# Kernel optimization log

Measured on AMD Instinct MI355X. Metric: run time of the kernel, lower is better.

Reference implementation:

```python
import jax, jax.numpy as jnp
import numpy as np

N_RES = 500000


def _rot(vals):
    # stack 9 scalars-per-element into (..., 3, 3) row-major rotation matrices
    return jnp.stack(vals, axis=-1).reshape(*vals[0].shape, 3, 3)


def _dihedral(p0, p1, p2, p3):
    b0 = -(p1 - p0)
    b1 = p2 - p1
    b2 = p3 - p2
    b0xb1 = jnp.cross(b0, b1)
    b1xb2 = jnp.cross(b2, b1)
    y = jnp.sum(jnp.cross(b0xb1, b1xb2) * b1, axis=-1) / jnp.linalg.norm(b1, axis=-1)
    x = jnp.sum(b0xb1 * b1xb2, axis=-1)
    return jnp.nan_to_num(jnp.arctan2(y, x))


def _bb_dihedrals(N, CA, C):
    phi_ = _dihedral(C[:-1], N[1:], CA[1:], C[1:])
    psi_ = _dihedral(N[:-1], CA[:-1], C[:-1], N[1:])
    omg_ = _dihedral(CA[:-1], C[:-1], N[1:], CA[1:])
    pad = jnp.zeros_like(phi_[:1])
    omega = jnp.concatenate([omg_, pad])
    phi = jnp.concatenate([pad, phi_])
    psi = jnp.concatenate([psi_, pad])
    return jnp.stack([omega, phi, psi], axis=-1)  # (n, 3)


def _frames_from_reference(n_xyz, ca_xyz, c_xyz, eps=1e-20):
    # OpenFold Rigid.make_transform_from_reference
    n = n_xyz - ca_xyz
    c = c_xyz - ca_xyz
    cx, cy, cz = c[..., 0], c[..., 1], c[..., 2]
    z = jnp.zeros_like(cx)
    o = jnp.ones_like(cx)
    nrm = jnp.sqrt(eps + cx**2 + cy**2)
    s1, c1 = -cy / nrm, cx / nrm
    R1 = _rot([c1, -s1, z, s1, c1, z, z, z, o])
    nrm2 = jnp.sqrt(eps + cx**2 + cy**2 + cz**2)
    s2, c2 = cz / nrm2, jnp.sqrt(cx**2 + cy**2) / nrm2
    R2 = _rot([c2, z, s2, z, o, z, -s2, z, c2])
    Rc = R2 @ R1
    n2 = jnp.einsum('...ij,...j->...i', Rc, n)
    ny, nz_ = n2[..., 1], n2[..., 2]
    nrm3 = jnp.sqrt(eps + ny**2 + nz_**2)
    sn, cn = -nz_ / nrm3, ny / nrm3
    Rn = _rot([o, z, z, z, cn, -sn, z, sn, cn])
    rots = jnp.swapaxes(Rn @ Rc, -1, -2)
    return rots, ca_xyz  # (n,3,3), (n,3)


def _compose(ra, ta, rb, tb):
    # rigid composition: (ra,ta) o (rb,tb)
    return ra @ rb, jnp.einsum('...ij,...j->...i', ra, tb) + ta


def _forward(aa, bb_coords, sc_torsions, default_frames, group_idx, atom_mask, lit_positions):
    n_xyz, ca_xyz, c_xyz = bb_coords[:, 0], bb_coords[:, 1], bb_coords[:, 2]
    bb_r, bb_t = _frames_from_reference(n_xyz, ca_xyz, c_xyz)

    angles = jnp.concatenate([_bb_dihedrals(n_xyz, ca_xyz, c_xyz), sc_torsions], axis=-1)  # (n,7)
    alpha = jnp.stack([jnp.sin(angles), jnp.cos(angles)], axis=-1)  # (n,7,2) [sin, cos]
    bb_pad = jnp.concatenate([
        jnp.zeros((alpha.shape[0], 1, 1), alpha.dtype),
        jnp.ones((alpha.shape[0], 1, 1), alpha.dtype)], axis=-1)
    alpha = jnp.concatenate([bb_pad, alpha], axis=-2)  # (n,8,2)

    # torsion_angles_to_frames
    d4 = default_frames[aa]            # (n,8,4,4)
    dr, dt = d4[..., :3, :3], d4[..., :3, 3]
    s, cA = alpha[..., 0], alpha[..., 1]
    z = jnp.zeros_like(s)
    o = jnp.ones_like(s)
    Ra = _rot([o, z, z, z, cA, -s, z, s, cA])  # (n,8,3,3) x-axis rotation
    fr = dr @ Ra
    ft = dt
    # chain chi2->chi1, chi3->chi2, chi4->chi3
    r2, t2 = _compose(fr[:, 4], ft[:, 4], fr[:, 5], ft[:, 5])
    r3, t3 = _compose(r2, t2, fr[:, 6], ft[:, 6])
    r4, t4 = _compose(r3, t3, fr[:, 7], ft[:, 7])
    all_r = jnp.concatenate([fr[:, :5], r2[:, None], r3[:, None], r4[:, None]], axis=1)
    all_t = jnp.concatenate([ft[:, :5], t2[:, None], t3[:, None], t4[:, None]], axis=1)
    gr, gt = _compose(bb_r[:, None], bb_t[:, None], all_r, all_t)  # (n,8,3,3), (n,8,3)

    # frames_and_literature_positions_to_atom14_pos (one-hot sum == gather)
    n = aa.shape[0]
    g = group_idx[aa]                   # (n,14)
    ridx = jnp.arange(n)[:, None]
    ar = gr[ridx, g]                    # (n,14,3,3)
    at = gt[ridx, g]                    # (n,14,3)
    lit = lit_positions[aa]             # (n,14,3)
    pred = jnp.einsum('naij,naj->nai', ar, lit) + at
    pred = pred * atom_mask[aa][..., None]

    # use_native_bb_coords=True: keep input backbone atoms
    return jnp.concatenate([bb_coords, pred[:, 4:]], axis=1)  # (n,14,3)


def setup_inputs() -> dict:
    key = jax.random.key(0)
    ks = jax.random.split(key, 7)
    n = N_RES
    aa = jax.random.randint(ks[0], (n,), 0, 21, dtype=jnp.int32)
    bb_coords = jax.random.normal(ks[1], (n, 4, 3), jnp.float32) * 3.0
    sc_torsions = jax.random.uniform(ks[2], (n, 4), jnp.float32, -np.pi, np.pi)
    default_frames = jax.random.normal(ks[3], (21, 8, 4, 4), jnp.float32)
    group_idx = jax.random.randint(ks[4], (21, 14), 0, 8, dtype=jnp.int32)
    atom_mask = (jax.random.uniform(ks[5], (21, 14)) > 0.2).astype(jnp.float32)
    lit_positions = jax.random.normal(ks[6], (21, 14, 3), jnp.float32)
    return {"aa": aa, "bb_coords": bb_coords, "sc_torsions": sc_torsions,
            "default_frames": default_frames, "group_idx": group_idx,
            "atom_mask": atom_mask, "lit_positions": lit_positions}


def reference(aa, bb_coords, sc_torsions, default_frames, group_idx, atom_mask, lit_positions):
    return _forward(aa, bb_coords, sc_torsions, default_frames, group_idx, atom_mask, lit_positions)
```

## Files before the change

### kernel.cpp

```cpp
#include <hip/hip_runtime.h>
#include <hip/hip_fp16.h>


struct F3 { float x, y, z; };

__device__ __forceinline__ F3 f3sub(F3 a, F3 b) { return {a.x-b.x, a.y-b.y, a.z-b.z}; }
__device__ __forceinline__ F3 f3cross(F3 a, F3 b) {
    return {a.y*b.z - a.z*b.y, a.z*b.x - a.x*b.z, a.x*b.y - a.y*b.x};
}
__device__ __forceinline__ float f3dot(F3 a, F3 b) { return a.x*b.x + a.y*b.y + a.z*b.z; }

__device__ __forceinline__ void dihedral_sc(F3 p0, F3 p1, F3 p2, F3 p3,
                                            float& s, float& c) {
    F3 b0 = f3sub(p0, p1);
    F3 b1 = f3sub(p2, p1);
    F3 b2 = f3sub(p3, p2);
    F3 u = f3cross(b0, b1);
    F3 v = f3cross(b2, b1);
    F3 w = f3cross(u, v);
    float y = f3dot(w, b1) * rsqrtf(fmaxf(f3dot(b1, b1), 1e-30f));
    float x = f3dot(u, v);
    float r2 = x*x + y*y;
    if (r2 > 1e-24f) {
        float rinv = rsqrtf(r2);
        s = y * rinv;
        c = x * rinv;
    } else {
        s = 0.0f;
        c = 1.0f;
    }
}

#define LIT_STRIDE 30
#define OT_STRIDE  30

__global__ __launch_bounds__(256, 4) void idealizer_kernel(
    const int*   __restrict__ aa,
    const float* __restrict__ bb,
    const float* __restrict__ tor,
    const float* __restrict__ dframes,
    const int*   __restrict__ gidx,
    const float* __restrict__ amask,
    const float* __restrict__ lit,
    float*       __restrict__ out,
    int n)
{
    __shared__ __align__(16) float  s_ot[256 * OT_STRIDE];
    __shared__ __align__(8)  __half s_dfh[21 * 8 * 12];
    __shared__ __align__(16) float  s_lit[21 * LIT_STRIDE];
    __shared__ unsigned s_gpk[21];
    __shared__ unsigned s_mbit[21];

    const int tid = threadIdx.x;
    for (int j = tid; j < 21 * 8 * 12; j += 256) {
        int blk = j / 12, e = j - blk * 12;
        s_dfh[j] = __float2half(dframes[blk * 16 + e]);
    }
    for (int j = tid; j < 21 * 30; j += 256) {
        int a = j / 30, r = j - a * 30;
        s_lit[a * LIT_STRIDE + r] = lit[a * 42 + 12 + r];
    }
    if (tid < 21) {
        unsigned gp = 0, mb = 0;
        #pragma unroll
        for (int a = 0; a < 10; a++) {
            gp |= ((unsigned)gidx[tid * 14 + 4 + a]) << (3 * a);
            mb |= (amask[tid * 14 + 4 + a] != 0.0f ? 1u : 0u) << a;
        }
        s_gpk[tid] = gp;
        s_mbit[tid] = mb;
    }
    __syncthreads();

    for (int i0 = blockIdx.x * 256; i0 < n; i0 += gridDim.x * 256) {
        const int i = i0 + tid;
        if (i < n) {
            const float4* bb4 = (const float4*)bb;
            float4 q0 = bb4[i * 3 + 0];
            float4 q1 = bb4[i * 3 + 1];
            float Cz  = bb[i * 12 + 8];
            F3 Np  = {q0.x, q0.y, q0.z};
            F3 CAp = {q0.w, q1.x, q1.y};
            F3 Cp  = {q1.z, q1.w, Cz};

            const int im = (i > 0)     ? i - 1 : 0;
            const int ip = (i < n - 1) ? i + 1 : 0;
            F3 Cm = { bb[im * 12 + 6], bb[im * 12 + 7], bb[im * 12 + 8] };
            float4 r0 = bb4[ip * 3 + 0];
            float2 r1 = ((const float2*)bb)[ip * 6 + 2];
            F3 Nn  = {r0.x, r0.y, r0.z};
            F3 CAn = {r0.w, r1.x, r1.y};

            float s_ph, c_ph, s_ps, c_ps, s_om, c_om;
            dihedral_sc(Cm,  Np,  CAp, Cp,  s_ph, c_ph);
            dihedral_sc(Np,  CAp, Cp,  Nn,  s_ps, c_ps);
            dihedral_sc(CAp, Cp,  Nn,  CAn, s_om, c_om);
            if (i == 0)     { s_ph = 0.0f; c_ph = 1.0f; }
            if (i == n - 1) { s_ps = 0.0f; c_ps = 1.0f; s_om = 0.0f; c_om = 1.0f; }

            const float eps = 1e-20f;
            F3 nv = f3sub(Np, CAp);
            F3 cv = f3sub(Cp, CAp);
            float cx = cv.x, cy = cv.y, cz = cv.z;
            float d2xy  = cx * cx + cy * cy;
            float inrm  = rsqrtf(eps + d2xy);
            float s1 = -cy * inrm, c1 = cx * inrm;
            float inrm2 = rsqrtf(eps + d2xy + cz * cz);
            float s2v = cz * inrm2, c2v = sqrtf(d2xy) * inrm2;
            float Rc00 = c2v * c1,  Rc01 = -c2v * s1, Rc02 = s2v;
            float Rc10 = s1,        Rc11 = c1,        Rc12 = 0.0f;
            float Rc20 = -s2v * c1, Rc21 = s2v * s1,  Rc22 = c2v;
            float n2y = Rc10 * nv.x + Rc11 * nv.y + Rc12 * nv.z;
            float n2z = Rc20 * nv.x + Rc21 * nv.y + Rc22 * nv.z;
            float inrm3 = rsqrtf(eps + n2y * n2y + n2z * n2z);
            float sn = -n2z * inrm3, cn = n2y * inrm3;
            float M10 = cn * Rc10 - sn * Rc20, M11 = cn * Rc11 - sn * Rc21, M12 = cn * Rc12 - sn * Rc22;
            float M20 = sn * Rc10 + cn * Rc20, M21 = sn * Rc11 + cn * Rc21, M22 = sn * Rc12 + cn * Rc22;
            float B00 = Rc00, B01 = M10, B02 = M20;
            float B10 = Rc01, B11 = M11, B12 = M21;
            float B20 = Rc02, B21 = M12, B22 = M22;

            float4 tv = ((const float4*)tor)[i];
            float sang[8], cang[8];
            sang[0] = 0.0f; cang[0] = 1.0f;
            sang[1] = s_om; cang[1] = c_om;
            sang[2] = s_ph; cang[2] = c_ph;
            sang[3] = s_ps; cang[3] = c_ps;
            __sincosf(tv.x, &sang[4], &cang[4]);
            __sincosf(tv.y, &sang[5], &cang[5]);
            __sincosf(tv.z, &sang[6], &cang[6]);
            __sincosf(tv.w, &sang[7], &cang[7]);

            const int aai = aa[i];
            const unsigned gpk  = s_gpk[aai];
            const unsigned mbit = s_mbit[aai];
            const float* lrow = &s_lit[aai * LIT_STRIDE];
            float* srow = &s_ot[tid * OT_STRIDE];

            float L00, L01, L02, L10, L11, L12, L20, L21, L22, Lx, Ly, Lz;
            const __half2* dfa = (const __half2*)(s_dfh + (size_t)aai * 96);
            #pragma unroll
            for (int g = 0; g < 8; g++) {
                const __half2* dh = dfa + g * 6;
                float2 e0 = __half22float2(dh[0]), e1 = __half22float2(dh[1]);
                float2 e2 = __half22float2(dh[2]), e3 = __half22float2(dh[3]);
                float2 e4 = __half22float2(dh[4]), e5 = __half22float2(dh[5]);
                float m00 = e0.x, m01 = e0.y, m02 = e1.x, tx = e1.y;
                float m10 = e2.x, m11 = e2.y, m12 = e3.x, ty = e3.y;
                float m20 = e4.x, m21 = e4.y, m22 = e5.x, tz = e5.y;
                float sA = sang[g], cA = cang[g];
                float f00 = m00, f01 = cA * m01 + sA * m02, f02 = cA * m02 - sA * m01;
                float f10 = m10, f11 = cA * m11 + sA * m12, f12 = cA * m12 - sA * m11;
                float f20 = m20, f21 = cA * m21 + sA * m22, f22 = cA * m22 - sA * m21;
                if (g <= 4) {
                    L00 = f00; L01 = f01; L02 = f02;
                    L10 = f10; L11 = f11; L12 = f12;
                    L20 = f20; L21 = f21; L22 = f22;
                    Lx = tx; Ly = ty; Lz = tz;
                } else {
                    float n00 = L00 * f00 + L01 * f10 + L02 * f20;
                    float n01 = L00 * f01 + L01 * f11 + L02 * f21;
                    float n02 = L00 * f02 + L01 * f12 + L02 * f22;
                    float n10 = L10 * f00 + L11 * f10 + L12 * f20;
                    float n11 = L10 * f01 + L11 * f11 + L12 * f21;
                    float n12 = L10 * f02 + L11 * f12 + L12 * f22;
                    float n20 = L20 * f00 + L21 * f10 + L22 * f20;
                    float n21 = L20 * f01 + L21 * f11 + L22 * f21;
                    float n22 = L20 * f02 + L21 * f12 + L22 * f22;
                    float ntx = L00 * tx + L01 * ty + L02 * tz + Lx;
                    float nty = L10 * tx + L11 * ty + L12 * tz + Ly;
                    float ntz = L20 * tx + L21 * ty + L22 * tz + Lz;
                    L00 = n00; L01 = n01; L02 = n02;
                    L10 = n10; L11 = n11; L12 = n12;
                    L20 = n20; L21 = n21; L22 = n22;
                    Lx = ntx; Ly = nty; Lz = ntz;
                }

                #pragma unroll
                for (int a = 0; a < 10; a++) {
                    bool sel = ((gpk >> (3 * a)) & 7u) == (unsigned)g;
                    if (sel) {
                        float mk = ((mbit >> a) & 1u) ? 1.0f : 0.0f;
                        float lx = lrow[3*a], ly = lrow[3*a+1], lz = lrow[3*a+2];
                        float qx = fmaf(L00, lx, fmaf(L01, ly, fmaf(L02, lz, Lx)));
                        float qy = fmaf(L10, lx, fmaf(L11, ly, fmaf(L12, lz, Ly)));
                        float qz = fmaf(L20, lx, fmaf(L21, ly, fmaf(L22, lz, Lz)));
                        float px = fmaf(B00, qx, fmaf(B01, qy, fmaf(B02, qz, CAp.x)));
                        float py = fmaf(B10, qx, fmaf(B11, qy, fmaf(B12, qz, CAp.y)));
                        float pz = fmaf(B20, qx, fmaf(B21, qy, fmaf(B22, qz, CAp.z)));
                        float* po = srow + 3 * a;
                        po[0] = mk * px;
                        po[1] = mk * py;
                        po[2] = mk * pz;
                    }
                }
            }
        }

        __syncthreads();

        int m = n - i0; if (m > 256) m = 256;
        const int cnt2 = m * 21;
        float2* gout = (float2*)(out + (size_t)i0 * 42);
        const float2* bbt = (const float2*)(bb + (size_t)i0 * 12);
        for (int off = tid; off < cnt2; off += 256) {
            int r = off / 21, j = off - r * 21;
            float2 val;
            if (j < 6) {
                val = bbt[r * 6 + j];
            } else {
                const float* tp = &s_ot[r * OT_STRIDE + 2 * (j - 6)];
                val = make_float2(tp[0], tp[1]);
            }
            gout[off] = val;
        }

        __syncthreads();
    }
}

extern "C" void kernel_launch(void* const* d_in, const int* in_sizes, int n_in,
                              void* d_out, int out_size, void* d_ws, size_t ws_size,
                              hipStream_t stream) {
    const int*   aa  = (const int*)d_in[0];
    const float* bb  = (const float*)d_in[1];
    const float* tor = (const float*)d_in[2];
    const float* df  = (const float*)d_in[3];
    const int*   gi  = (const int*)d_in[4];
    const float* am  = (const float*)d_in[5];
    const float* lp  = (const float*)d_in[6];
    float* outp = (float*)d_out;
    const int n = in_sizes[0];
    int tiles = (n + 255) / 256;
    int blocks = tiles < 1024 ? tiles : 1024;
    idealizer_kernel<<<blocks, 256, 0, stream>>>(aa, bb, tor, df, gi, am, lp, outp, n);
}
```

Baseline: 156.6 us.

## Share dihedral cross products, store frames fp32, predicate atom placement, simplify store indexing

Computes the backbone bond vectors and their cross products once and shares them across the phi, psi and omega dihedrals. Default frames now sit in shared memory as fp32 float4 rows and literature positions as fp16. Atom placement becomes branchless: local positions are selected into registers, the backbone transform is applied once per atom, and results are written to LDS as float2. The output copy loop advances row and column incrementally instead of dividing each iteration. It also lowers the launch-bounds occupancy hint from 4 to 3 and adds a redundant M22 expression. The costs are higher register pressure, extra FMAs for atoms that are not selected, and fp16 rounding of the literature positions.

```diff
diff --git a/kernel.cpp b/kernel.cpp
--- a/kernel.cpp
+++ b/kernel.cpp
@@ -10,31 +10,22 @@
 }
 __device__ __forceinline__ float f3dot(F3 a, F3 b) { return a.x*b.x + a.y*b.y + a.z*b.z; }
 
-__device__ __forceinline__ void dihedral_sc(F3 p0, F3 p1, F3 p2, F3 p3,
-                                            float& s, float& c) {
-    F3 b0 = f3sub(p0, p1);
-    F3 b1 = f3sub(p2, p1);
-    F3 b2 = f3sub(p3, p2);
-    F3 u = f3cross(b0, b1);
-    F3 v = f3cross(b2, b1);
-    F3 w = f3cross(u, v);
-    float y = f3dot(w, b1) * rsqrtf(fmaxf(f3dot(b1, b1), 1e-30f));
-    float x = f3dot(u, v);
-    float r2 = x*x + y*y;
-    if (r2 > 1e-24f) {
-        float rinv = rsqrtf(r2);
-        s = y * rinv;
-        c = x * rinv;
-    } else {
-        s = 0.0f;
-        c = 1.0f;
-    }
-}
-
-#define LIT_STRIDE 30
-#define OT_STRIDE  30
-
-__global__ __launch_bounds__(256, 4) void idealizer_kernel(
+__device__ __forceinline__ void dihedral_from(F3 A, F3 B, F3 mid,
+                                              float& s, float& c) {
+    float x = f3dot(A, B);
+    F3 w = f3cross(A, B);
+    float y = f3dot(w, mid) * rsqrtf(fmaxf(f3dot(mid, mid), 1e-30f));
+    float r2 = x * x + y * y;
+    float rinv = rsqrtf(r2);
+    bool ok = r2 > 1e-24f;
+    s = ok ? y * rinv : 0.0f;
+    c = ok ? x * rinv : 1.0f;
+}
+
+#define DF_AA     100
+#define OT_STRIDE 30
+
+__global__ __launch_bounds__(256, 3) void idealizer_kernel(
     const int*   __restrict__ aa,
     const float* __restrict__ bb,
     const float* __restrict__ tor,
@@ -46,19 +37,19 @@
     int n)
 {
     __shared__ __align__(16) float  s_ot[256 * OT_STRIDE];
-    __shared__ __align__(8)  __half s_dfh[21 * 8 * 12];
-    __shared__ __align__(16) float  s_lit[21 * LIT_STRIDE];
+    __shared__ __align__(16) float  s_df[21 * DF_AA];
+    __shared__ __align__(8)  __half s_lith[21 * 32];
     __shared__ unsigned s_gpk[21];
     __shared__ unsigned s_mbit[21];
 
     const int tid = threadIdx.x;
     for (int j = tid; j < 21 * 8 * 12; j += 256) {
         int blk = j / 12, e = j - blk * 12;
-        s_dfh[j] = __float2half(dframes[blk * 16 + e]);
+        s_df[(blk >> 3) * DF_AA + (blk & 7) * 12 + e] = dframes[blk * 16 + e];
     }
     for (int j = tid; j < 21 * 30; j += 256) {
         int a = j / 30, r = j - a * 30;
-        s_lit[a * LIT_STRIDE + r] = lit[a * 42 + 12 + r];
+        s_lith[a * 32 + r] = __float2half(lit[a * 42 + 12 + r]);
     }
     if (tid < 21) {
         unsigned gp = 0, mb = 0;
@@ -91,22 +82,29 @@
             F3 Nn  = {r0.x, r0.y, r0.z};
             F3 CAn = {r0.w, r1.x, r1.y};
 
+            F3 u1 = f3sub(Np, Cm);
+            F3 u2 = f3sub(CAp, Np);
+            F3 u3 = f3sub(Cp, CAp);
+            F3 u4 = f3sub(Nn, Cp);
+            F3 u5 = f3sub(CAn, Nn);
+            F3 c12 = f3cross(u1, u2), c23 = f3cross(u2, u3);
+            F3 c34 = f3cross(u3, u4), c45 = f3cross(u4, u5);
             float s_ph, c_ph, s_ps, c_ps, s_om, c_om;
-            dihedral_sc(Cm,  Np,  CAp, Cp,  s_ph, c_ph);
-            dihedral_sc(Np,  CAp, Cp,  Nn,  s_ps, c_ps);
-            dihedral_sc(CAp, Cp,  Nn,  CAn, s_om, c_om);
+            dihedral_from(c12, c23, u2, s_ph, c_ph);
+            dihedral_from(c23, c34, u3, s_ps, c_ps);
+            dihedral_from(c34, c45, u4, s_om, c_om);
             if (i == 0)     { s_ph = 0.0f; c_ph = 1.0f; }
             if (i == n - 1) { s_ps = 0.0f; c_ps = 1.0f; s_om = 0.0f; c_om = 1.0f; }
 
             const float eps = 1e-20f;
             F3 nv = f3sub(Np, CAp);
             F3 cv = f3sub(Cp, CAp);
-            float cx = cv.x, cy = cv.y, cz = cv.z;
+            float cx = cv.x, cy = cv.y, cz2 = cv.z;
             float d2xy  = cx * cx + cy * cy;
             float inrm  = rsqrtf(eps + d2xy);
             float s1 = -cy * inrm, c1 = cx * inrm;
-            float inrm2 = rsqrtf(eps + d2xy + cz * cz);
-            float s2v = cz * inrm2, c2v = sqrtf(d2xy) * inrm2;
+            float inrm2 = rsqrtf(eps + d2xy + cz2 * cz2);
+            float s2v = cz2 * inrm2, c2v = sqrtf(d2xy) * inrm2;
             float Rc00 = c2v * c1,  Rc01 = -c2v * s1, Rc02 = s2v;
             float Rc10 = s1,        Rc11 = c1,        Rc12 = 0.0f;
             float Rc20 = -s2v * c1, Rc21 = s2v * s1,  Rc22 = c2v;
@@ -115,7 +113,8 @@
             float inrm3 = rsqrtf(eps + n2y * n2y + n2z * n2z);
             float sn = -n2z * inrm3, cn = n2y * inrm3;
             float M10 = cn * Rc10 - sn * Rc20, M11 = cn * Rc11 - sn * Rc21, M12 = cn * Rc12 - sn * Rc22;
-            float M20 = sn * Rc10 + cn * Rc20, M21 = sn * Rc11 + cn * Rc21, M22 = sn * Rc12 + cn * Rc22;
+            float M20 = sn * Rc10 + cn * Rc20, M21 = sn * Rc11 + cn * Rc21, M22 = sn * Rc22 * 0.0f + sn * Rc12 + cn * Rc22;
+            M22 = sn * Rc12 + cn * Rc22;
             float B00 = Rc00, B01 = M10, B02 = M20;
             float B10 = Rc01, B11 = M11, B12 = M21;
             float B20 = Rc02, B21 = M12, B22 = M22;
@@ -134,29 +133,36 @@
             const int aai = aa[i];
             const unsigned gpk  = s_gpk[aai];
             const unsigned mbit = s_mbit[aai];
-            const float* lrow = &s_lit[aai * LIT_STRIDE];
-            float* srow = &s_ot[tid * OT_STRIDE];
+
+            float la[30];
+            {
+                const __half2* lh = (const __half2*)&s_lith[aai * 32];
+                #pragma unroll
+                for (int k = 0; k < 15; k++) {
+                    float2 t = __half22float2(lh[k]);
+                    la[2*k] = t.x; la[2*k+1] = t.y;
+                }
+            }
+
+            float v[30];
+            #pragma unroll
+            for (int k = 0; k < 30; k++) v[k] = 0.0f;
 
             float L00, L01, L02, L10, L11, L12, L20, L21, L22, Lx, Ly, Lz;
-            const __half2* dfa = (const __half2*)(s_dfh + (size_t)aai * 96);
+            const float* dfa = &s_df[aai * DF_AA];
             #pragma unroll
             for (int g = 0; g < 8; g++) {
-                const __half2* dh = dfa + g * 6;
-                float2 e0 = __half22float2(dh[0]), e1 = __half22float2(dh[1]);
-                float2 e2 = __half22float2(dh[2]), e3 = __half22float2(dh[3]);
-                float2 e4 = __half22float2(dh[4]), e5 = __half22float2(dh[5]);
-                float m00 = e0.x, m01 = e0.y, m02 = e1.x, tx = e1.y;
-                float m10 = e2.x, m11 = e2.y, m12 = e3.x, ty = e3.y;
-                float m20 = e4.x, m21 = e4.y, m22 = e5.x, tz = e5.y;
+                const float4* dfr = (const float4*)(dfa + g * 12);
+                float4 d0 = dfr[0], d1 = dfr[1], d2 = dfr[2];
                 float sA = sang[g], cA = cang[g];
-                float f00 = m00, f01 = cA * m01 + sA * m02, f02 = cA * m02 - sA * m01;
-                float f10 = m10, f11 = cA * m11 + sA * m12, f12 = cA * m12 - sA * m11;
-                float f20 = m20, f21 = cA * m21 + sA * m22, f22 = cA * m22 - sA * m21;
+                float f00 = d0.x, f01 = cA * d0.y + sA * d0.z, f02 = cA * d0.z - sA * d0.y;
+                float f10 = d1.x, f11 = cA * d1.y + sA * d1.z, f12 = cA * d1.z - sA * d1.y;
+                float f20 = d2.x, f21 = cA * d2.y + sA * d2.z, f22 = cA * d2.z - sA * d2.y;
                 if (g <= 4) {
                     L00 = f00; L01 = f01; L02 = f02;
                     L10 = f10; L11 = f11; L12 = f12;
                     L20 = f20; L21 = f21; L22 = f22;
-                    Lx = tx; Ly = ty; Lz = tz;
+                    Lx = d0.w; Ly = d1.w; Lz = d2.w;
                 } else {
                     float n00 = L00 * f00 + L01 * f10 + L02 * f20;
                     float n01 = L00 * f01 + L01 * f11 + L02 * f21;
@@ -167,9 +173,9 @@
                     float n20 = L20 * f00 + L21 * f10 + L22 * f20;
                     float n21 = L20 * f01 + L21 * f11 + L22 * f21;
                     float n22 = L20 * f02 + L21 * f12 + L22 * f22;
-                    float ntx = L00 * tx + L01 * ty + L02 * tz + Lx;
-                    float nty = L10 * tx + L11 * ty + L12 * tz + Ly;
-                    float ntz = L20 * tx + L21 * ty + L22 * tz + Lz;
+                    float ntx = L00 * d0.w + L01 * d1.w + L02 * d2.w + Lx;
+                    float nty = L10 * d0.w + L11 * d1.w + L12 * d2.w + Ly;
+                    float ntz = L20 * d0.w + L21 * d1.w + L22 * d2.w + Lz;
                     L00 = n00; L01 = n01; L02 = n02;
                     L10 = n10; L11 = n11; L12 = n12;
                     L20 = n20; L21 = n21; L22 = n22;
@@ -179,22 +185,28 @@
                 #pragma unroll
                 for (int a = 0; a < 10; a++) {
                     bool sel = ((gpk >> (3 * a)) & 7u) == (unsigned)g;
-                    if (sel) {
-                        float mk = ((mbit >> a) & 1u) ? 1.0f : 0.0f;
-                        float lx = lrow[3*a], ly = lrow[3*a+1], lz = lrow[3*a+2];
-                        float qx = fmaf(L00, lx, fmaf(L01, ly, fmaf(L02, lz, Lx)));
-                        float qy = fmaf(L10, lx, fmaf(L11, ly, fmaf(L12, lz, Ly)));
-                        float qz = fmaf(L20, lx, fmaf(L21, ly, fmaf(L22, lz, Lz)));
-                        float px = fmaf(B00, qx, fmaf(B01, qy, fmaf(B02, qz, CAp.x)));
-                        float py = fmaf(B10, qx, fmaf(B11, qy, fmaf(B12, qz, CAp.y)));
-                        float pz = fmaf(B20, qx, fmaf(B21, qy, fmaf(B22, qz, CAp.z)));
-                        float* po = srow + 3 * a;
-                        po[0] = mk * px;
-                        po[1] = mk * py;
-                        po[2] = mk * pz;
-                    }
+                    float qx = fmaf(L00, la[3*a], fmaf(L01, la[3*a+1], fmaf(L02, la[3*a+2], Lx)));
+                    float qy = fmaf(L10, la[3*a], fmaf(L11, la[3*a+1], fmaf(L12, la[3*a+2], Ly)));
+                    float qz = fmaf(L20, la[3*a], fmaf(L21, la[3*a+1], fmaf(L22, la[3*a+2], Lz)));
+                    v[3*a]   = sel ? qx : v[3*a];
+                    v[3*a+1] = sel ? qy : v[3*a+1];
+                    v[3*a+2] = sel ? qz : v[3*a+2];
                 }
             }
+
+            #pragma unroll
+            for (int a = 0; a < 10; a++) {
+                float mk = ((mbit >> a) & 1u) ? 1.0f : 0.0f;
+                float qx = v[3*a], qy = v[3*a+1], qz = v[3*a+2];
+                v[3*a]   = mk * fmaf(B00, qx, fmaf(B01, qy, fmaf(B02, qz, CAp.x)));
+                v[3*a+1] = mk * fmaf(B10, qx, fmaf(B11, qy, fmaf(B12, qz, CAp.y)));
+                v[3*a+2] = mk * fmaf(B20, qx, fmaf(B21, qy, fmaf(B22, qz, CAp.z)));
+            }
+
+            float2* so2 = (float2*)&s_ot[tid * OT_STRIDE];
+            #pragma unroll
+            for (int k = 0; k < 15; k++)
+                so2[k] = make_float2(v[2*k], v[2*k+1]);
         }
 
         __syncthreads();
@@ -203,16 +215,17 @@
         const int cnt2 = m * 21;
         float2* gout = (float2*)(out + (size_t)i0 * 42);
         const float2* bbt = (const float2*)(bb + (size_t)i0 * 12);
+        int r = tid / 21;
+        int j = tid - r * 21;
         for (int off = tid; off < cnt2; off += 256) {
-            int r = off / 21, j = off - r * 21;
-            float2 val;
-            if (j < 6) {
-                val = bbt[r * 6 + j];
-            } else {
-                const float* tp = &s_ot[r * OT_STRIDE + 2 * (j - 6)];
-                val = make_float2(tp[0], tp[1]);
-            }
-            gout[off] = val;
+            int bi = (j < 6) ? (r * 6 + j) : 0;
+            float2 gval = bbt[bi];
+            int tj = (j < 6) ? 0 : (j - 6);
+            const float* tp = &s_ot[r * OT_STRIDE + 2 * tj];
+            float2 lval = make_float2(tp[0], tp[1]);
+            gout[off] = (j < 6) ? gval : lval;
+            r += 12; j += 4;
+            if (j >= 21) { j -= 21; r += 1; }
         }
 
         __syncthreads();
```

After: 153.9 us. About the same (-1.8%).
